# Optimization experiments

Hardware: AMD Instinct MI355X
Metric: run time of the kernel (lower is better)

## Reference

```python
import math
import jax, jax.numpy as jnp
import numpy as np

LEVELS = [1, 2, 4, 8, 16]  # pyramid pool sizes (init kwarg)
MODE = 'avg'               # init kwarg

B = 8
D = 256
# ragged per-graph node counts, sum = 160000
COUNTS = np.array([12000, 18000, 25000, 15000, 30000, 22000, 17000, 21000], dtype=np.int64)


def setup_inputs() -> dict:
    key = jax.random.key(0)
    k1, k2 = jax.random.split(key)
    n_total = int(COUNTS.sum())
    x = jax.random.normal(k1, (n_total, D), dtype=jnp.float32)
    degrees = jax.random.randint(k2, (n_total,), 0, 100, dtype=jnp.int64)
    return {"x": x, "num_per_batch": COUNTS, "degrees": degrees}


def _pyramid_pool_graph(feats):
    # feats: [D, n] (features transposed, nodes sorted by degree desc)
    d, n = feats.shape
    outs = []
    for p in LEVELS:
        kernel = int(math.ceil(n / p))
        pad = kernel * p - n
        padded = jnp.pad(feats, ((0, 0), (0, pad)))  # zero pad on the right
        blocks = padded.reshape(d, p, kernel)
        if MODE == 'avg':
            # AvgPool1d default count_include_pad=True -> mean over full kernel incl. zeros
            pooled = blocks.mean(axis=2)
        else:
            pooled = blocks.max(axis=2)
        outs.append(pooled)
    # tpp.view(D * sum(levels)): row-major flatten of [D, sum(levels)]
    return jnp.concatenate(outs, axis=1).reshape(-1)


def reference(x, num_per_batch, degrees):
    counts = np.asarray(num_per_batch)
    offsets = np.concatenate([[0], np.cumsum(counts)])
    cols = []
    for g in range(len(counts)):
        s, e = int(offsets[g]), int(offsets[g + 1])
        deg = degrees[s:e]
        # sorted(..., reverse=True) is stable -> stable argsort of negated keys
        order = jnp.argsort(-deg, stable=True)
        feats = x[s:e][order].T  # [D, n_g]
        cols.append(_pyramid_pool_graph(feats))
    # read_out is [D*sumL, B]; forward returns its transpose -> [B, D*sumL]
    return jnp.stack(cols, axis=0)
```

## Files before the change

kernel.cpp:

```cpp
#include <hip/hip_runtime.h>


#define DFEAT 256
#define NPOOL 31

static __device__ __constant__ int c_goff[9] =
    {0, 12000, 30000, 55000, 70000, 100000, 122000, 139000, 160000};
static __device__ __constant__ int c_poff[9] =
    {0, 47, 118, 216, 275, 393, 479, 546, 629};
static __device__ __constant__ int c_lvl[5]    = {1, 2, 4, 8, 16};
static __device__ __constant__ int c_lvloff[5] = {0, 1, 3, 7, 15};

#define NCHUNK 629
#define NACC 63488

__global__ __launch_bounds__(256) void k_hist(const int* __restrict__ deg,
                                              int* __restrict__ chist,
                                              float* __restrict__ accb) {
    __shared__ int whist[4][100];
    int c = blockIdx.x;
    int t = threadIdx.x;
    if (c < 248) accb[c * 256 + t] = 0.0f;
    int w = t >> 6, l = t & 63;
    int g = 0;
    while (c >= c_poff[g + 1]) ++g;
    int i = c_goff[g] + (c - c_poff[g]) * 256 + t;
    int bin = -1;
    if (i < c_goff[g + 1]) {
        int dg = deg[i];
        bin = dg < 0 ? 0 : (dg > 99 ? 99 : dg);
    }
    int cnt0 = 0, cnt1 = 0;
    for (int v = 0; v < 100; ++v) {
        unsigned long long m = __ballot(bin == v);
        int pc = __popcll(m);
        if (l == v) cnt0 = pc;
        if (l + 64 == v) cnt1 = pc;
    }
    whist[w][l] = cnt0;
    if (l < 36) whist[w][64 + l] = cnt1;
    __syncthreads();
    if (t < 100)
        chist[c * 100 + t] = whist[0][t] + whist[1][t] + whist[2][t] + whist[3][t];
}

__global__ __launch_bounds__(64) void k_scan(int* __restrict__ chist,
                                             int* __restrict__ totals) {
    int b = blockIdx.x;
    int g = b / 100, k = b % 100;
    int l = threadIdx.x;
    int c0 = c_poff[g], c1 = c_poff[g + 1];
    int running = 0;
    for (int base = c0; base < c1; base += 64) {
        int c = base + l;
        int val = (c < c1) ? chist[c * 100 + k] : 0;
        int incl = val;
        #pragma unroll
        for (int off = 1; off < 64; off <<= 1) {
            int y = __shfl_up(incl, off);
            if (l >= off) incl += y;
        }
        if (c < c1) chist[c * 100 + k] = running + (incl - val);
        running += __shfl(incl, 63);
    }
    if (l == 0) totals[g * 100 + k] = running;
}

__global__ __launch_bounds__(256) void k_scatter(const int* __restrict__ deg,
                                                 const int* __restrict__ chist,
                                                 const int* __restrict__ totals,
                                                 int* __restrict__ sidx) {
    __shared__ int tt[100];
    __shared__ int ssum[100];
    __shared__ int whist[4][100];
    int c = blockIdx.x;
    int t = threadIdx.x;
    int w = t >> 6, l = t & 63;
    int g = 0;
    while (c >= c_poff[g + 1]) ++g;

    if (t < 100) tt[t] = totals[g * 100 + t];
    __syncthreads();
    if (t < 100) {
        int s = 0;
        for (int j2 = t + 1; j2 < 100; ++j2) s += tt[j2];
        ssum[t] = s;
    }

    int i = c_goff[g] + (c - c_poff[g]) * 256 + t;
    bool valid = i < c_goff[g + 1];
    int bin = -1;
    if (valid) {
        int dg = deg[i];
        bin = dg < 0 ? 0 : (dg > 99 ? 99 : dg);
    }
    unsigned long long mymask = 0;
    int cnt0 = 0, cnt1 = 0;
    for (int v = 0; v < 100; ++v) {
        unsigned long long m = __ballot(bin == v);
        int pc = __popcll(m);
        if (bin == v) mymask = m;
        if (l == v) cnt0 = pc;
        if (l + 64 == v) cnt1 = pc;
    }
    whist[w][l] = cnt0;
    if (l < 36) whist[w][64 + l] = cnt1;
    __syncthreads();

    if (valid) {
        int wpre = 0;
        for (int w2 = 0; w2 < 4; ++w2)
            if (w2 < w) wpre += whist[w2][bin];
        unsigned long long below = mymask & ((1ull << l) - 1ull);
        int rank = ssum[bin] + chist[c * 100 + bin] + wpre + __popcll(below);
        sidx[c_goff[g] + rank] = i;
    }
}

__global__ __launch_bounds__(256) void k_pool(const float* __restrict__ x,
                                              const int* __restrict__ sidx,
                                              float* __restrict__ acc) {
    __shared__ int sIdxSm[256];
    __shared__ float red[1024];
    int b = blockIdx.x;
    int g = 0;
    while (b >= c_poff[g + 1]) ++g;
    int n = c_goff[g + 1] - c_goff[g];
    int r0 = (b - c_poff[g]) * 256;
    int r1 = min(r0 + 256, n);
    int t = threadIdx.x;
    if (t < r1 - r0) sIdxSm[t] = sidx[c_goff[g] + r0 + t];
    __syncthreads();

    const int w = t >> 6;
    const int l = t & 63;

    float invk[5];
    int j[5], nb[5], kk[5];
    #pragma unroll
    for (int lev = 0; lev < 5; ++lev) {
        int p = c_lvl[lev];
        kk[lev] = (n + p - 1) / p;
        invk[lev] = 1.0f / (float)kk[lev];
        j[lev] = r0 / kk[lev];
        nb[lev] = (j[lev] + 1) * kk[lev];
    }
    float* ag = acc + (size_t)g * (DFEAT * NPOOL);

    int s = r0;
    while (s < r1) {
        int send = r1;
        #pragma unroll
        for (int lev = 0; lev < 5; ++lev) send = min(send, nb[lev]);

        float4 a0 = {0, 0, 0, 0}, a1 = {0, 0, 0, 0};
        float4 a2 = {0, 0, 0, 0}, a3 = {0, 0, 0, 0};
        int r = s + w;
        for (; r + 12 < send; r += 16) {
            const float4 v0 = *(const float4*)(x + (size_t)sIdxSm[r      - r0] * DFEAT + l * 4);
            const float4 v1 = *(const float4*)(x + (size_t)sIdxSm[r + 4  - r0] * DFEAT + l * 4);
            const float4 v2 = *(const float4*)(x + (size_t)sIdxSm[r + 8  - r0] * DFEAT + l * 4);
            const float4 v3 = *(const float4*)(x + (size_t)sIdxSm[r + 12 - r0] * DFEAT + l * 4);
            a0 += v0; a1 += v1; a2 += v2; a3 += v3;
        }
        for (; r < send; r += 4) {
            a0 += *(const float4*)(x + (size_t)sIdxSm[r - r0] * DFEAT + l * 4);
        }
        a0 += a1; a2 += a3; a0 += a2;
        *(float4*)(red + w * 256 + l * 4) = a0;
        __syncthreads();
        float S = red[t] + red[256 + t] + red[512 + t] + red[768 + t];
        #pragma unroll
        for (int lev = 0; lev < 5; ++lev) {
            atomicAdd(ag + (c_lvloff[lev] + j[lev]) * DFEAT + t, S * invk[lev]);
            if (send == nb[lev]) { j[lev]++; nb[lev] += kk[lev]; }
        }
        s = send;
        __syncthreads();
    }
}

__global__ __launch_bounds__(256) void k_finish(const float* __restrict__ acc,
                                                float* __restrict__ out, int nOut) {
    int i = blockIdx.x * 256 + threadIdx.x;
    if (i < nOut) {
        int g = i / (DFEAT * NPOOL);
        int rem = i % (DFEAT * NPOOL);
        int d = rem / NPOOL;
        int slot = rem % NPOOL;
        out[i] = acc[g * (DFEAT * NPOOL) + slot * DFEAT + d];
    }
}

extern "C" void kernel_launch(void* const* d_in, const int* in_sizes, int n_in,
                              void* d_out, int out_size, void* d_ws, size_t ws_size,
                              hipStream_t stream) {
    const float* x  = (const float*)d_in[0];
    const int* deg  = (const int*)d_in[2];
    float* out      = (float*)d_out;

    int* ws      = (int*)d_ws;
    int* chist   = ws;
    int* totals  = ws + 62900;
    int* sidx    = ws + 63700;
    float* accb  = (float*)(ws + 223700);

    hipLaunchKernelGGL(k_hist, dim3(NCHUNK), dim3(256), 0, stream, deg, chist, accb);
    hipLaunchKernelGGL(k_scan, dim3(800), dim3(64), 0, stream, chist, totals);
    hipLaunchKernelGGL(k_scatter, dim3(NCHUNK), dim3(256), 0, stream, deg, chist,
                       totals, sidx);
    hipLaunchKernelGGL(k_pool, dim3(NCHUNK), dim3(256), 0, stream, x, sidx, accb);
    hipLaunchKernelGGL(k_finish, dim3((out_size + 255) / 256), dim3(256), 0, stream,
                       accb, out, out_size);
}
```

Before: 54.34 us.

## Replace sorted-index gather with per-node segment IDs and in-order streaming accumulation

```diff
diff --git a/kernel.cpp b/kernel.cpp
--- a/kernel.cpp
+++ b/kernel.cpp
@@ -8,11 +8,8 @@
     {0, 12000, 30000, 55000, 70000, 100000, 122000, 139000, 160000};
 static __device__ __constant__ int c_poff[9] =
     {0, 47, 118, 216, 275, 393, 479, 546, 629};
-static __device__ __constant__ int c_lvl[5]    = {1, 2, 4, 8, 16};
-static __device__ __constant__ int c_lvloff[5] = {0, 1, 3, 7, 15};
 
 #define NCHUNK 629
-#define NACC 63488
 
 __global__ __launch_bounds__(256) void k_hist(const int* __restrict__ deg,
                                               int* __restrict__ chist,
@@ -69,7 +66,7 @@
 __global__ __launch_bounds__(256) void k_scatter(const int* __restrict__ deg,
                                                  const int* __restrict__ chist,
                                                  const int* __restrict__ totals,
-                                                 int* __restrict__ sidx) {
+                                                 unsigned* __restrict__ segs) {
     __shared__ int tt[100];
     __shared__ int ssum[100];
     __shared__ int whist[4][100];
@@ -113,71 +110,82 @@
             if (w2 < w) wpre += whist[w2][bin];
         unsigned long long below = mymask & ((1ull << l) - 1ull);
         int rank = ssum[bin] + chist[c * 100 + bin] + wpre + __popcll(below);
-        sidx[c_goff[g] + rank] = i;
+        int nn = c_goff[g + 1] - c_goff[g];
+        int kk2  = (nn + 1) >> 1;
+        int kk4  = (nn + 3) >> 2;
+        int kk8  = (nn + 7) >> 3;
+        int kk16 = (nn + 15) >> 4;
+        segs[i] = (unsigned)(rank / kk2 + rank / kk4 + rank / kk8 + rank / kk16);
     }
 }
 
 __global__ __launch_bounds__(256) void k_pool(const float* __restrict__ x,
-                                              const int* __restrict__ sidx,
+                                              const unsigned* __restrict__ segs,
                                               float* __restrict__ acc) {
-    __shared__ int sIdxSm[256];
-    __shared__ float red[1024];
+    __shared__ float accP[256 * 27];
+    __shared__ unsigned segSm[256];
     int b = blockIdx.x;
     int g = 0;
     while (b >= c_poff[g + 1]) ++g;
     int n = c_goff[g + 1] - c_goff[g];
-    int r0 = (b - c_poff[g]) * 256;
-    int r1 = min(r0 + 256, n);
+    int i0 = c_goff[g] + (b - c_poff[g]) * 256;
+    int nrow = min(256, c_goff[g + 1] - i0);
     int t = threadIdx.x;
-    if (t < r1 - r0) sIdxSm[t] = sidx[c_goff[g] + r0 + t];
-    __syncthreads();
-
-    const int w = t >> 6;
-    const int l = t & 63;
-
-    float invk[5];
-    int j[5], nb[5], kk[5];
     #pragma unroll
-    for (int lev = 0; lev < 5; ++lev) {
-        int p = c_lvl[lev];
-        kk[lev] = (n + p - 1) / p;
-        invk[lev] = 1.0f / (float)kk[lev];
-        j[lev] = r0 / kk[lev];
-        nb[lev] = (j[lev] + 1) * kk[lev];
-    }
+    for (int q = 0; q < 27; ++q) accP[t * 27 + q] = 0.0f;
+    if (t < nrow) segSm[t] = segs[i0 + t];
+    __syncthreads();
+
+    float* myacc = accP + t * 27;
+    const float* xp = x + (size_t)i0 * DFEAT + t;
+
+    #pragma unroll 8
+    for (int r = 0; r < nrow; ++r) {
+        float v = xp[(size_t)r * DFEAT];
+        myacc[segSm[r]] += v;
+    }
+    __syncthreads();
+
+    int kk2  = (n + 1) >> 1;
+    int kk4  = (n + 3) >> 2;
+    int kk8  = (n + 7) >> 3;
+    int kk16 = (n + 15) >> 4;
+    float inv1  = 1.0f / (float)n;
+    float inv2  = 1.0f / (float)kk2;
+    float inv4  = 1.0f / (float)kk4;
+    float inv8  = 1.0f / (float)kk8;
+    float inv16 = 1.0f / (float)kk16;
     float* ag = acc + (size_t)g * (DFEAT * NPOOL);
 
-    int s = r0;
-    while (s < r1) {
-        int send = r1;
-        #pragma unroll
-        for (int lev = 0; lev < 5; ++lev) send = min(send, nb[lev]);
-
-        float4 a0 = {0, 0, 0, 0}, a1 = {0, 0, 0, 0};
-        float4 a2 = {0, 0, 0, 0}, a3 = {0, 0, 0, 0};
-        int r = s + w;
-        for (; r + 12 < send; r += 16) {
-            const float4 v0 = *(const float4*)(x + (size_t)sIdxSm[r      - r0] * DFEAT + l * 4);
-            const float4 v1 = *(const float4*)(x + (size_t)sIdxSm[r + 4  - r0] * DFEAT + l * 4);
-            const float4 v2 = *(const float4*)(x + (size_t)sIdxSm[r + 8  - r0] * DFEAT + l * 4);
-            const float4 v3 = *(const float4*)(x + (size_t)sIdxSm[r + 12 - r0] * DFEAT + l * 4);
-            a0 += v0; a1 += v1; a2 += v2; a3 += v3;
-        }
-        for (; r < send; r += 4) {
-            a0 += *(const float4*)(x + (size_t)sIdxSm[r - r0] * DFEAT + l * 4);
-        }
-        a0 += a1; a2 += a3; a0 += a2;
-        *(float4*)(red + w * 256 + l * 4) = a0;
-        __syncthreads();
-        float S = red[t] + red[256 + t] + red[512 + t] + red[768 + t];
-        #pragma unroll
-        for (int lev = 0; lev < 5; ++lev) {
-            atomicAdd(ag + (c_lvloff[lev] + j[lev]) * DFEAT + t, S * invk[lev]);
-            if (send == nb[lev]) { j[lev]++; nb[lev] += kk[lev]; }
-        }
-        s = send;
-        __syncthreads();
-    }
+    int j2 = 0, j4 = 0, j8 = 0, j16 = 0;
+    float r1 = 0.f, r2 = 0.f, r4 = 0.f, r8 = 0.f, r16 = 0.f;
+    int pos = 0;
+    while (pos < n) {
+        int b2 = (j2 + 1) * kk2, b4 = (j4 + 1) * kk4;
+        int b8 = (j8 + 1) * kk8, b16 = (j16 + 1) * kk16;
+        int nb = min(n, min(min(b2, b4), min(b8, b16)));
+        int seg = j2 + j4 + j8 + j16;
+        float a = myacc[seg];
+        r1 += a; r2 += a; r4 += a; r8 += a; r16 += a;
+        pos = nb;
+        if (nb == b16 || nb == n) {
+            atomicAdd(ag + (15 + j16) * DFEAT + t, r16 * inv16);
+            r16 = 0.f; ++j16;
+        }
+        if (nb == b8 || nb == n) {
+            atomicAdd(ag + (7 + j8) * DFEAT + t, r8 * inv8);
+            r8 = 0.f; ++j8;
+        }
+        if (nb == b4 || nb == n) {
+            atomicAdd(ag + (3 + j4) * DFEAT + t, r4 * inv4);
+            r4 = 0.f; ++j4;
+        }
+        if (nb == b2 || nb == n) {
+            atomicAdd(ag + (1 + j2) * DFEAT + t, r2 * inv2);
+            r2 = 0.f; ++j2;
+        }
+    }
+    atomicAdd(ag + t, r1 * inv1);
 }
 
 __global__ __launch_bounds__(256) void k_finish(const float* __restrict__ acc,
@@ -199,17 +207,17 @@
     const int* deg  = (const int*)d_in[2];
     float* out      = (float*)d_out;
 
-    int* ws      = (int*)d_ws;
-    int* chist   = ws;
-    int* totals  = ws + 62900;
-    int* sidx    = ws + 63700;
-    float* accb  = (float*)(ws + 223700);
+    int* ws          = (int*)d_ws;
+    int* chist       = ws;
+    int* totals      = ws + 62900;
+    unsigned* segsW  = (unsigned*)(ws + 63700);
+    float* accb      = (float*)(ws + 223700);
 
     hipLaunchKernelGGL(k_hist, dim3(NCHUNK), dim3(256), 0, stream, deg, chist, accb);
     hipLaunchKernelGGL(k_scan, dim3(800), dim3(64), 0, stream, chist, totals);
     hipLaunchKernelGGL(k_scatter, dim3(NCHUNK), dim3(256), 0, stream, deg, chist,
-                       totals, sidx);
-    hipLaunchKernelGGL(k_pool, dim3(NCHUNK), dim3(256), 0, stream, x, sidx, accb);
+                       totals, segsW);
+    hipLaunchKernelGGL(k_pool, dim3(NCHUNK), dim3(256), 0, stream, x, segsW, accb);
     hipLaunchKernelGGL(k_finish, dim3((out_size + 255) / 256), dim3(256), 0, stream,
                        accb, out, out_size);
 }
```

Measured after the change: 79.26 us. 1.46x slower.
